# Performance work log

Measured on AMD Instinct MI355X. Metric: run time of the kernel, lower is better.

## Reference

```python
import jax, jax.numpy as jnp
import numpy as np

TEMPERATURE = 0.5
BN_EPS = 1e-5
L2_EPS = 1e-12

B, D_IN, D_HID, D_OUT = 4096, 192, 512, 128


def setup_inputs() -> dict:
    key = jax.random.key(0)
    ks = jax.random.split(key, 4)
    return {
        "h1": jax.random.normal(ks[0], (B, D_IN), dtype=jnp.float32),
        "h2": jax.random.normal(ks[1], (B, D_IN), dtype=jnp.float32),
        "W1": jax.random.normal(ks[2], (D_HID, D_IN), dtype=jnp.float32) * (1.0 / np.sqrt(D_IN)),
        "b1": jnp.zeros((D_HID,), dtype=jnp.float32),
        "gamma": jnp.ones((D_HID,), dtype=jnp.float32),
        "beta": jnp.zeros((D_HID,), dtype=jnp.float32),
        "W2": jax.random.normal(ks[3], (D_OUT, D_HID), dtype=jnp.float32) * (1.0 / np.sqrt(D_HID)),
        "b2": jnp.zeros((D_OUT,), dtype=jnp.float32),
    }


def _projection_head(h, W1, b1, gamma, beta, W2, b2):
    # Linear -> BatchNorm1d (training-mode batch stats) -> ReLU -> Linear
    y = h @ W1.T + b1  # (B, D_HID)
    mean = jnp.mean(y, axis=0)
    var = jnp.mean((y - mean) ** 2, axis=0)  # biased var, as torch BN uses for normalization
    y = (y - mean) * jax.lax.rsqrt(var + BN_EPS) * gamma + beta
    y = jax.nn.relu(y)
    return y @ W2.T + b2  # (B, D_OUT)


def _l2_normalize(z):
    n = jnp.sqrt(jnp.sum(z * z, axis=1, keepdims=True))
    return z / jnp.maximum(n, L2_EPS)


def reference(h1, h2, W1, b1, gamma, beta, W2, b2):
    z1 = _l2_normalize(_projection_head(h1, W1, b1, gamma, beta, W2, b2))
    z2 = _l2_normalize(_projection_head(h2, W1, b1, gamma, beta, W2, b2))

    # NT-Xent, fully vectorized (equivalent to the per-row torch loop):
    z = jnp.concatenate([z1, z2], axis=0)            # (2B, D)
    sim = (z @ z.T) / TEMPERATURE                    # (2B, 2B)
    n2 = z.shape[0]
    sim = jnp.where(jnp.eye(n2, dtype=bool), -jnp.inf, sim)
    # positive pair similarity: sim[i, i+B] and sim[i+B, i] == z1_i . z2_i / T
    pos = jnp.sum(z1 * z2, axis=1) / TEMPERATURE     # (B,)
    pos = jnp.concatenate([pos, pos])                # (2B,)
    # excluding index i from the row equals including it since diag is -inf
    lse = jax.nn.logsumexp(sim, axis=1)              # (2B,)
    loss = jnp.mean(lse - pos)
    return loss, z1, z2
```

## Files before the change

kernel.cpp:

```cpp
#include <hip/hip_runtime.h>


#define NB   4096
#define DIN  192
#define DHID 512
#define DOUT 128
#define N2   8192
#define NSPLIT 64
#define SIM_TILES 8

typedef short short8 __attribute__((ext_vector_type(8)));
typedef float floatx4 __attribute__((ext_vector_type(4)));

__device__ inline float fast_exp2(float x) {
#if __has_builtin(__builtin_amdgcn_exp2f)
    return __builtin_amdgcn_exp2f(x);
#else
    return exp2f(x);
#endif
}

__device__ inline unsigned short bf16_rne(float x) {
    unsigned int u = __float_as_uint(x);
    return (unsigned short)((u + 0x7fffu + ((u >> 16) & 1u)) >> 16);
}

__global__ __launch_bounds__(256) void prep(
    const float* __restrict__ W1, const float* __restrict__ W2,
    unsigned short* __restrict__ W1b, unsigned short* __restrict__ W2b,
    float* __restrict__ psumc, float* __restrict__ psqc, float* __restrict__ out)
{
    const int NW1 = DHID * DIN / 4;
    const int NW2 = DOUT * DHID / 4;
    if (blockIdx.x == 160) {
        int t = threadIdx.x;
        for (int i = t; i < 1024; i += 256) { psumc[i] = 0.f; psqc[i] = 0.f; }
        if (t == 0) out[0] = 0.f;
        return;
    }
    int id = blockIdx.x * 256 + threadIdx.x;
    const float* src; unsigned short* dst; int off;
    if (id < NW1)            { src = W1; dst = W1b; off = id; }
    else if (id < NW1 + NW2) { src = W2; dst = W2b; off = id - NW1; }
    else return;
    float4 x = ((const float4*)src)[off];
    unsigned int p0 = bf16_rne(x.x) | ((unsigned int)bf16_rne(x.y) << 16);
    unsigned int p1 = bf16_rne(x.z) | ((unsigned int)bf16_rne(x.w) << 16);
    ((uint2*)dst)[off] = make_uint2(p0, p1);
}

__global__ __launch_bounds__(256) void gemm1_mfma(
    const float* __restrict__ h1, const float* __restrict__ h2,
    const unsigned short* __restrict__ W1b, const float* __restrict__ b1,
    float* __restrict__ Y, float* __restrict__ psumc, float* __restrict__ psqc)
{
    const int t = threadIdx.x;
    const int wave = t >> 6, lane = t & 63;
    const int quad = lane >> 4, l15 = lane & 15;
    const int mb = blockIdx.x;
    const int m0 = mb * 128 + wave * 32;
    const int n0 = blockIdx.y * 64;
    const int v  = (mb >= 32);

    short8 a[2][6];
    #pragma unroll
    for (int mt = 0; mt < 2; ++mt) {
        int row = m0 + mt * 16 + l15;
        const float* hsrc = (row < NB) ? (h1 + (size_t)row * DIN)
                                       : (h2 + (size_t)(row - NB) * DIN);
        #pragma unroll
        for (int kc = 0; kc < 6; ++kc) {
            const float4* p = (const float4*)(hsrc + kc * 32 + quad * 8);
            float4 x0 = p[0], x1 = p[1];
            float xs[8] = {x0.x,x0.y,x0.z,x0.w,x1.x,x1.y,x1.z,x1.w};
            #pragma unroll
            for (int j = 0; j < 8; ++j) a[mt][kc][j] = (short)bf16_rne(xs[j]);
        }
    }

    #pragma unroll
    for (int nt = 0; nt < 4; ++nt) {
        const int col = n0 + nt * 16 + l15;
        const short8* bptr = (const short8*)(W1b + (size_t)col * DIN + quad * 8);
        short8 b[6];
        #pragma unroll
        for (int kc = 0; kc < 6; ++kc) b[kc] = bptr[kc * 4];
        floatx4 acc[2] = {{0.f,0.f,0.f,0.f},{0.f,0.f,0.f,0.f}};
        #pragma unroll
        for (int kc = 0; kc < 6; ++kc)
            #pragma unroll
            for (int mt = 0; mt < 2; ++mt)
                acc[mt] = __builtin_amdgcn_mfma_f32_16x16x32_bf16(a[mt][kc], b[kc], acc[mt], 0,0,0);
        const float bias = b1[col];
        float cs = 0.f, cq = 0.f;
        #pragma unroll
        for (int mt = 0; mt < 2; ++mt)
            #pragma unroll
            for (int reg = 0; reg < 4; ++reg) {
                float y = acc[mt][reg] + bias;
                int row = m0 + mt * 16 + quad * 4 + reg;
                Y[(size_t)row * DHID + col] = y;
                cs += y; cq += y * y;
            }
        cs += __shfl_xor(cs, 16); cs += __shfl_xor(cs, 32);
        cq += __shfl_xor(cq, 16); cq += __shfl_xor(cq, 32);
        if (quad == 0) {
            atomicAdd(psumc + v * DHID + col, cs);
            atomicAdd(psqc  + v * DHID + col, cq);
        }
    }
}

#define ZSCALE 1.6986436f

__global__ __launch_bounds__(256) void gemm2_mfma(
    const float* __restrict__ Y, const unsigned short* __restrict__ W2b,
    const float* __restrict__ psumc, const float* __restrict__ psqc,
    const float* __restrict__ gamma, const float* __restrict__ beta,
    const float* __restrict__ b2,
    unsigned short* __restrict__ Zb, float* __restrict__ outz)
{
    __shared__ float sc_sh[DHID], sh_sh[DHID];
    __shared__ float sq_lds[4][16];
    const int t = threadIdx.x;
    const int wave = t >> 6, lane = t & 63;
    const int quad = lane >> 4, l15 = lane & 15;
    const int mtbase = blockIdx.x * 16;
    const int v = (mtbase >= NB);

    for (int c = t; c < DHID; c += 256) {
        float mean = psumc[v * DHID + c] * (1.0f / NB);
        float var  = psqc [v * DHID + c] * (1.0f / NB) - mean * mean;
        float rstd = rsqrtf(var + 1e-5f);
        float scv = gamma[c] * rstd;
        sc_sh[c] = scv;
        sh_sh[c] = beta[c] - mean * scv;
    }
    __syncthreads();

    const float* yrow = Y + (size_t)(mtbase + l15) * DHID;
    floatx4 acc[2] = {{0.f,0.f,0.f,0.f},{0.f,0.f,0.f,0.f}};
    for (int kc = 0; kc < 16; ++kc) {
        const int k = kc * 32 + quad * 8;
        float4 y0 = *(const float4*)(yrow + k);
        float4 y1 = *(const float4*)(yrow + k + 4);
        float4 s0 = *(const float4*)&sc_sh[k], s1 = *(const float4*)&sc_sh[k + 4];
        float4 h0 = *(const float4*)&sh_sh[k], h1v = *(const float4*)&sh_sh[k + 4];
        float xs[8];
        xs[0] = fmaxf(y0.x * s0.x + h0.x, 0.f);
        xs[1] = fmaxf(y0.y * s0.y + h0.y, 0.f);
        xs[2] = fmaxf(y0.z * s0.z + h0.z, 0.f);
        xs[3] = fmaxf(y0.w * s0.w + h0.w, 0.f);
        xs[4] = fmaxf(y1.x * s1.x + h1v.x, 0.f);
        xs[5] = fmaxf(y1.y * s1.y + h1v.y, 0.f);
        xs[6] = fmaxf(y1.z * s1.z + h1v.z, 0.f);
        xs[7] = fmaxf(y1.w * s1.w + h1v.w, 0.f);
        short8 a;
        #pragma unroll
        for (int j = 0; j < 8; ++j) a[j] = (short)bf16_rne(xs[j]);
        #pragma unroll
        for (int nt = 0; nt < 2; ++nt) {
            const int col = wave * 32 + nt * 16 + l15;
            short8 b = *(const short8*)(W2b + (size_t)col * DHID + k);
            acc[nt] = __builtin_amdgcn_mfma_f32_16x16x32_bf16(a, b, acc[nt], 0,0,0);
        }
    }
    float bias[2];
    #pragma unroll
    for (int nt = 0; nt < 2; ++nt) bias[nt] = b2[wave * 32 + nt * 16 + l15];

    float zv[4][2];
    #pragma unroll
    for (int reg = 0; reg < 4; ++reg) {
        float sq = 0.f;
        #pragma unroll
        for (int nt = 0; nt < 2; ++nt) {
            zv[reg][nt] = acc[nt][reg] + bias[nt];
            sq += zv[reg][nt] * zv[reg][nt];
        }
        sq += __shfl_xor(sq, 1); sq += __shfl_xor(sq, 2);
        sq += __shfl_xor(sq, 4); sq += __shfl_xor(sq, 8);
        if (l15 == 0) sq_lds[wave][quad * 4 + reg] = sq;
    }
    __syncthreads();
    #pragma unroll
    for (int reg = 0; reg < 4; ++reg) {
        float tot = sq_lds[0][quad * 4 + reg] + sq_lds[1][quad * 4 + reg]
                  + sq_lds[2][quad * 4 + reg] + sq_lds[3][quad * 4 + reg];
        float inv = 1.0f / fmaxf(sqrtf(tot), 1e-12f);
        const int row = mtbase + quad * 4 + reg;
        const size_t ob = (size_t)row * DOUT;
        #pragma unroll
        for (int nt = 0; nt < 2; ++nt) {
            const int col = wave * 32 + nt * 16 + l15;
            float z = zv[reg][nt] * inv;
            outz[ob + col] = z;
            Zb[ob + col] = bf16_rne(z * ZSCALE);
        }
    }
}

__global__ __launch_bounds__(256, 4) void sim_mfma(
    const unsigned short* __restrict__ Zb, float* __restrict__ psum)
{
    __shared__ unsigned char bsh[32768];
    const int t = threadIdx.x;
    const int wave = t >> 6, lane = t & 63;
    const int quad = lane >> 4, l15 = lane & 15;
    const int cs = blockIdx.y;
    const int cbase = cs * (N2 / NSPLIT);

    {
        const uint4* src = (const uint4*)(Zb + (size_t)cbase * DOUT);
        #pragma unroll
        for (int k = 0; k < 8; ++k) {
            int idx = t + k * 256;
            uint4 vv = src[idx];
            int row  = idx >> 4;
            int slot = idx & 15;
            *(uint4*)(bsh + row * 256 + ((slot ^ (row & 15)) << 4)) = vv;
        }
    }
    __syncthreads();

    #pragma unroll 1
    for (int g = 0; g < 4; ++g) {
        const int mbase = blockIdx.x * 512 + g * 128 + wave * 32;

        short8 a[2][4];
        #pragma unroll
        for (int at = 0; at < 2; ++at) {
            const short8* zra = (const short8*)(Zb + (size_t)(mbase + at * 16 + l15) * DOUT + quad * 8);
            #pragma unroll
            for (int kc = 0; kc < 4; ++kc) a[at][kc] = zra[kc * 4];
        }

        float rs[2][4];
        #pragma unroll
        for (int at = 0; at < 2; ++at)
            #pragma unroll
            for (int r = 0; r < 4; ++r) rs[at][r] = 0.f;

        #pragma unroll 1
        for (int np = 0; np < SIM_TILES / 2; ++np) {
            short8 b[2][4];
            #pragma unroll
            for (int j = 0; j < 2; ++j) {
                const int crow = (np * 2 + j) * 16 + l15;
                #pragma unroll
                for (int kc = 0; kc < 4; ++kc) {
                    int slot = kc * 4 + quad;
                    int boff = crow * 256 + ((slot ^ (crow & 15)) << 4);
                    b[j][kc] = *(const short8*)(bsh + boff);
                }
            }

            floatx4 acc[2][2] = {{{0.f,0.f,0.f,0.f},{0.f,0.f,0.f,0.f}},
                                 {{0.f,0.f,0.f,0.f},{0.f,0.f,0.f,0.f}}};
            #pragma unroll
            for (int kc = 0; kc < 4; ++kc)
                #pragma unroll
                for (int at = 0; at < 2; ++at)
                    #pragma unroll
                    for (int j = 0; j < 2; ++j)
                        acc[at][j] = __builtin_amdgcn_mfma_f32_16x16x32_bf16(a[at][kc], b[j][kc], acc[at][j], 0, 0, 0);

            #pragma unroll
            for (int at = 0; at < 2; ++at)
                #pragma unroll
                for (int r = 0; r < 4; ++r)
                    rs[at][r] += fast_exp2(acc[at][0][r]) + fast_exp2(acc[at][1][r]);
        }

        #pragma unroll
        for (int at = 0; at < 2; ++at) {
            const int gi0 = mbase + at * 16 + quad * 4;
            #pragma unroll
            for (int r = 0; r < 4; ++r) {
                float s = rs[at][r];
                s += __shfl_xor(s, 1);
                s += __shfl_xor(s, 2);
                s += __shfl_xor(s, 4);
                s += __shfl_xor(s, 8);
                if (l15 == 0) psum[(size_t)cs * N2 + gi0 + r] = s;
            }
        }
    }
}

__global__ __launch_bounds__(256) void row_finalize(
    const unsigned short* __restrict__ Zb, const float* __restrict__ psum,
    float* __restrict__ out)
{
    const int t = threadIdx.x, wave = t >> 6, lane = t & 63;
    const int half = lane >> 5, l5 = lane & 31;
    const unsigned int* Z32 = (const unsigned int*)Zb;
    const int gw = blockIdx.x * 4 + wave;
    float accrv = 0.f;

    #pragma unroll 1
    for (int pp = 0; pp < 4; ++pp) {
        const int k = gw * 4 + pp;
        const int idx = k + half * NB;
        float s = psum[(size_t)l5 * N2 + idx]
                + psum[(size_t)(l5 + 32) * N2 + idx];
        s += __shfl_xor(s, 1); s += __shfl_xor(s, 2); s += __shfl_xor(s, 4);
        s += __shfl_xor(s, 8); s += __shfl_xor(s, 16);
        unsigned int aw = Z32[(size_t)k * 64 + lane];
        unsigned int bw = Z32[(size_t)(k + NB) * 64 + lane];
        float alo = __uint_as_float(aw << 16), ahi = __uint_as_float(aw & 0xffff0000u);
        float blo = __uint_as_float(bw << 16), bhi = __uint_as_float(bw & 0xffff0000u);
        float d12 = alo * blo + ahi * bhi;
        float d11 = alo * alo + ahi * ahi;
        float d22 = blo * blo + bhi * bhi;
        #pragma unroll
        for (int m = 1; m <= 32; m <<= 1) {
            d12 += __shfl_xor(d12, m);
            d11 += __shfl_xor(d11, m);
            d22 += __shfl_xor(d22, m);
        }
        if (l5 == 0) {
            float dself = half ? d22 : d11;
            accrv += logf(s - fast_exp2(dself)) - d12 * 0.69314718f;
        }
    }
    accrv += __shfl_xor(accrv, 32);
    __shared__ float wsr[4];
    if (lane == 0) wsr[wave] = accrv;
    __syncthreads();
    if (t == 0)
        atomicAdd(out, (wsr[0] + wsr[1] + wsr[2] + wsr[3]) * (1.0f / N2));
}

extern "C" void kernel_launch(void* const* d_in, const int* in_sizes, int n_in,
                              void* d_out, int out_size, void* d_ws, size_t ws_size,
                              hipStream_t stream)
{
    const float* h1    = (const float*)d_in[0];
    const float* h2    = (const float*)d_in[1];
    const float* W1    = (const float*)d_in[2];
    const float* b1    = (const float*)d_in[3];
    const float* gamma = (const float*)d_in[4];
    const float* beta  = (const float*)d_in[5];
    const float* W2    = (const float*)d_in[6];
    const float* b2    = (const float*)d_in[7];
    float* out = (float*)d_out;

    float* ws      = (float*)d_ws;
    float* psumc   = ws;
    float* psqc    = psumc + 1024;
    unsigned short* W1b = (unsigned short*)(psqc + 1024);
    unsigned short* W2b = W1b + DHID * DIN;
    float* Y       = (float*)(W2b + DOUT * DHID);
    float* psum    = Y + (size_t)N2 * DHID;
    unsigned short* Zb = (unsigned short*)(psum + (size_t)NSPLIT * N2);

    prep        <<<dim3(161),        256, 0, stream>>>(W1, W2, W1b, W2b, psumc, psqc, out);
    gemm1_mfma  <<<dim3(64, 8),      256, 0, stream>>>(h1, h2, W1b, b1, Y, psumc, psqc);
    gemm2_mfma  <<<dim3(512),        256, 0, stream>>>(Y, W2b, psumc, psqc, gamma, beta, b2, Zb, out + 1);
    sim_mfma    <<<dim3(16, NSPLIT), 256, 0, stream>>>(Zb, psum);
    row_finalize<<<dim3(256),        256, 0, stream>>>(Zb, psum, out);
}
```

Measured before the change: 137.9 us.

## Exploit symmetry of similarity matrix to compute only upper-triangle tiles

The similarity kernel now skips 128x128 tiles below the diagonal. Each off-diagonal tile also accumulates column sums of exp(sim), combined in shared memory, and writes them as the partial sums for the transposed tile. This roughly halves the MFMA and exp work of the dominant kernel. In exchange it adds cross-lane shuffles, shared-memory accumulation and block barriers per tile, and early-exiting blocks leave the load unbalanced across the grid.

Result: slower. 147.0 us (+6.6%).

```diff
diff --git a/kernel.cpp b/kernel.cpp
--- a/kernel.cpp
+++ b/kernel.cpp
@@ -7,7 +7,6 @@
 #define DOUT 128
 #define N2   8192
 #define NSPLIT 64
-#define SIM_TILES 8
 
 typedef short short8 __attribute__((ext_vector_type(8)));
 typedef float floatx4 __attribute__((ext_vector_type(4)));
@@ -204,11 +203,15 @@
     const unsigned short* __restrict__ Zb, float* __restrict__ psum)
 {
     __shared__ unsigned char bsh[32768];
+    __shared__ float colsum[4][128];
     const int t = threadIdx.x;
     const int wave = t >> 6, lane = t & 63;
     const int quad = lane >> 4, l15 = lane & 15;
+    const int X  = blockIdx.x;
     const int cs = blockIdx.y;
-    const int cbase = cs * (N2 / NSPLIT);
+    if (cs < 4 * X) return;
+
+    const int cbase = cs * 128;
 
     {
         const uint4* src = (const uint4*)(Zb + (size_t)cbase * DOUT);
@@ -225,7 +228,15 @@
 
     #pragma unroll 1
     for (int g = 0; g < 4; ++g) {
-        const int mbase = blockIdx.x * 512 + g * 128 + wave * 32;
+        const int r = 4 * X + g;
+        if (cs < r) continue;
+        const bool diag = (cs == r);
+        const int mbase = r * 128 + wave * 32;
+
+        if (!diag) {
+            colsum[wave][lane] = 0.f;
+            colsum[wave][lane + 64] = 0.f;
+        }
 
         short8 a[2][4];
         #pragma unroll
@@ -239,10 +250,10 @@
         #pragma unroll
         for (int at = 0; at < 2; ++at)
             #pragma unroll
-            for (int r = 0; r < 4; ++r) rs[at][r] = 0.f;
+            for (int rr = 0; rr < 4; ++rr) rs[at][rr] = 0.f;
 
         #pragma unroll 1
-        for (int np = 0; np < SIM_TILES / 2; ++np) {
+        for (int np = 0; np < 4; ++np) {
             short8 b[2][4];
             #pragma unroll
             for (int j = 0; j < 2; ++j) {
@@ -266,24 +277,46 @@
                         acc[at][j] = __builtin_amdgcn_mfma_f32_16x16x32_bf16(a[at][kc], b[j][kc], acc[at][j], 0, 0, 0);
 
             #pragma unroll
-            for (int at = 0; at < 2; ++at)
+            for (int j = 0; j < 2; ++j) {
+                float cst = 0.f;
                 #pragma unroll
-                for (int r = 0; r < 4; ++r)
-                    rs[at][r] += fast_exp2(acc[at][0][r]) + fast_exp2(acc[at][1][r]);
+                for (int at = 0; at < 2; ++at)
+                    #pragma unroll
+                    for (int rr = 0; rr < 4; ++rr) {
+                        float e = fast_exp2(acc[at][j][rr]);
+                        rs[at][rr] += e;
+                        cst += e;
+                    }
+                if (!diag) {
+                    cst += __shfl_xor(cst, 16);
+                    cst += __shfl_xor(cst, 32);
+                    if (quad == 0) colsum[wave][(np * 2 + j) * 16 + l15] += cst;
+                }
+            }
         }
 
         #pragma unroll
         for (int at = 0; at < 2; ++at) {
             const int gi0 = mbase + at * 16 + quad * 4;
             #pragma unroll
-            for (int r = 0; r < 4; ++r) {
-                float s = rs[at][r];
+            for (int rr = 0; rr < 4; ++rr) {
+                float s = rs[at][rr];
                 s += __shfl_xor(s, 1);
                 s += __shfl_xor(s, 2);
                 s += __shfl_xor(s, 4);
                 s += __shfl_xor(s, 8);
-                if (l15 == 0) psum[(size_t)cs * N2 + gi0 + r] = s;
-            }
+                if (l15 == 0) psum[(size_t)cs * N2 + gi0 + rr] = s;
+            }
+        }
+
+        if (!diag) {
+            __syncthreads();
+            if (t < 128) {
+                float tot = colsum[0][t] + colsum[1][t]
+                          + colsum[2][t] + colsum[3][t];
+                psum[(size_t)r * N2 + cbase + t] = tot;
+            }
+            __syncthreads();
         }
     }
 }
```
